# Kernel optimization log

Measured on AMD Instinct MI355X. Metric: run time of the kernel, lower is better.

## Reference

```python
import math
import jax, jax.numpy as jnp
import numpy as np

FACTOR = 5


def setup_inputs() -> dict:
    key = jax.random.key(0)
    kq, kk, kv, ki = jax.random.split(key, 4)
    B, H, L, D = 4, 8, 2048, 64
    sample_k = min(FACTOR * math.ceil(math.log(L)), L)  # 40
    queries = jax.random.normal(kq, (B, H, L, D), dtype=jnp.float32)
    keys = jax.random.normal(kk, (B, H, L, D), dtype=jnp.float32)
    values = jax.random.normal(kv, (B, H, L, D), dtype=jnp.float32)
    index_sample = jax.random.randint(ki, (L, sample_k), 0, L, dtype=jnp.int64 if jax.config.jax_enable_x64 else jnp.int32)
    return {"queries": queries, "keys": keys, "values": values, "index_sample": index_sample}


def reference(queries, keys, values, index_sample):
    B, H, L_Q, D = queries.shape
    L_K = keys.shape[2]
    u = min(FACTOR * math.ceil(math.log(L_Q)), L_Q)  # n_top queries (= 40)
    scale = 1.0 / math.sqrt(D)

    # --- _prob_QK: sparsity measurement over randomly sampled keys ---
    # K_sample[b,h,q,s,:] = keys[b,h,index_sample[q,s],:]  -> [B,H,L_Q,S,D]
    K_sample = keys[:, :, index_sample, :]
    Q_K_sample = jnp.einsum('bhqd,bhqsd->bhqs', queries, K_sample)  # [B,H,L_Q,S]
    M = Q_K_sample.max(axis=-1) - Q_K_sample.sum(axis=-1) / L_K      # [B,H,L_Q]
    _, M_top = jax.lax.top_k(M, u)                                    # [B,H,u]

    Q_reduce = jnp.take_along_axis(queries, M_top[..., None], axis=2)  # [B,H,u,D]
    scores_top = jnp.einsum('bhud,bhkd->bhuk', Q_reduce, keys) * scale  # [B,H,u,L_K]

    # --- initial context: causal cumulative sum of V (mask_flag=True) ---
    context = jnp.cumsum(values, axis=2)  # [B,H,L_Q,D]

    # --- ProbMask: causal rows gathered at the selected query indices ---
    causal = jnp.triu(jnp.ones((L_Q, L_K), dtype=bool), 1)  # [L_Q,L_K]
    mask = causal[M_top]                                     # [B,H,u,L_K]
    scores_top = jnp.where(mask, -jnp.inf, scores_top)

    attn = jax.nn.softmax(scores_top, axis=-1)                       # [B,H,u,L_K]
    update = jnp.einsum('bhuk,bhkd->bhud', attn, values)             # [B,H,u,D]

    b_idx = jnp.arange(B)[:, None, None]
    h_idx = jnp.arange(H)[None, :, None]
    context = context.at[b_idx, h_idx, M_top].set(update.astype(context.dtype))
    return context
```

## Files before the change

kernel.cpp:

```cpp
#include <hip/hip_runtime.h>
#include <math.h>

#define BB 4
#define HH 8
#define LL 2048
#define DD 64
#define SK 40
#define BH (BB*HH)

__device__ __forceinline__ unsigned ordu(float v) {
    unsigned u = __float_as_uint(v);
    return (u & 0x80000000u) ? ~u : (u | 0x80000000u);
}

__global__ __launch_bounds__(256) void stage1_kernel(
        const float* __restrict__ Q, const float* __restrict__ K,
        const float* __restrict__ V, const int* __restrict__ IDX,
        float* __restrict__ M, float* __restrict__ csum) {
    int tid = threadIdx.x;
    if (blockIdx.x < 1024) {
        int x = blockIdx.x;
        int bhLo = x & 7;
        int r = x >> 3;
        int bhHi = r & 3;
        int chunk = r >> 2;
        int bh = bhHi * 8 + bhLo;
        int qbase = chunk * 64;
        int w = tid >> 6, lane = tid & 63;
        int qw = lane >> 2, c = lane & 3;
        int qi = w * 16 + qw;
        int qpos = qbase + qi;

        __shared__ int sidx[64 * SK];
        for (int i = tid; i < 64 * SK; i += 256) sidx[i] = IDX[(size_t)qbase * SK + i];

        const float4* Q4 = (const float4*)Q;
        const float4* K4 = (const float4*)K;
        float4 qreg[4];
        #pragma unroll
        for (int j = 0; j < 4; ++j)
            qreg[j] = Q4[((size_t)bh * LL + qpos) * 16 + j * 4 + c];
        __syncthreads();

        size_t kb4 = (size_t)bh * LL * 16;
        float mx = -INFINITY, sm = 0.f;
        #pragma unroll 8
        for (int s = 0; s < SK; ++s) {
            int ks = sidx[qi * SK + s];
            const float4* kr = K4 + kb4 + (size_t)ks * 16;
            float p = 0.f;
            #pragma unroll
            for (int j = 0; j < 4; ++j) {
                float4 kv = kr[j * 4 + c];
                p += qreg[j].x * kv.x + qreg[j].y * kv.y + qreg[j].z * kv.z + qreg[j].w * kv.w;
            }
            p += __shfl_xor(p, 1, 64);
            p += __shfl_xor(p, 2, 64);
            mx = fmaxf(mx, p);
            sm += p;
        }
        if (c == 0) M[(size_t)bh * LL + qpos] = mx - sm * (1.0f / (float)LL);
    } else {
        int x = blockIdx.x - 1024;
        int bhLo = x & 7, r = x >> 3;
        int bhHi = r & 3, c = r >> 2;
        int bh = bhHi * 8 + bhLo;
        int d = tid & 63, sg = tid >> 6;
        size_t base = (size_t)bh * LL * DD;
        int row0 = c * 128 + sg * 32;
        float s = 0.f;
        for (int j = 0; j < 32; ++j) s += V[base + (size_t)(row0 + j) * DD + d];
        __shared__ float part[4][DD];
        part[sg][d] = s;
        __syncthreads();
        if (sg == 0)
            csum[((size_t)bh * 16 + c) * DD + d] = part[0][d] + part[1][d] + part[2][d] + part[3][d];
    }
}

__global__ __launch_bounds__(256) void stage2_kernel(
        const float* __restrict__ V, const float* __restrict__ csum,
        const float* __restrict__ M, float* __restrict__ out,
        int* __restrict__ topk) {
    int tid = threadIdx.x;
    if (blockIdx.x < 512) {
        int x = blockIdx.x;
        int bhLo = x & 7, r = x >> 3;
        int bhHi = r & 3, c = r >> 2;
        int bh = bhHi * 8 + bhLo;
        int d = tid & 63, sg = tid >> 6;
        size_t base = (size_t)bh * LL * DD;
        int row0 = c * 128 + sg * 32;
        float v[32];
        #pragma unroll
        for (int j = 0; j < 32; ++j) v[j] = V[base + (size_t)(row0 + j) * DD + d];
        float s = 0.f;
        #pragma unroll
        for (int j = 0; j < 32; ++j) s += v[j];
        __shared__ float part[4][DD];
        part[sg][d] = s;
        __syncthreads();
        float pre = 0.f;
        for (int cc = 0; cc < c; ++cc) pre += csum[((size_t)bh * 16 + cc) * DD + d];
        for (int ss = 0; ss < sg; ++ss) pre += part[ss][d];
        float acc = pre;
        #pragma unroll
        for (int j = 0; j < 32; ++j) {
            acc += v[j];
            out[base + (size_t)(row0 + j) * DD + d] = acc;
        }
    } else {
        int bh = blockIdx.x - 512;
        __shared__ unsigned hist[256];
        __shared__ unsigned bc_prefix, bc_need;
        __shared__ unsigned cnt_gt, cnt_eq;
        __shared__ int eqlist[128];

        unsigned v[8];
        #pragma unroll
        for (int j = 0; j < 8; ++j)
            v[j] = ordu(M[(size_t)bh * LL + tid + j * 256]);

        unsigned prefix = 0, need = SK;
        #pragma unroll
        for (int pass = 0; pass < 4; ++pass) {
            const int s = 24 - 8 * pass;
            const unsigned maskHigh = (pass == 0) ? 0u : (0xFFFFFFFFu << (s + 8));
            hist[tid] = 0;
            __syncthreads();
            #pragma unroll
            for (int j = 0; j < 8; ++j)
                if (((v[j] ^ prefix) & maskHigh) == 0)
                    atomicAdd(&hist[(v[j] >> s) & 0xFF], 1u);
            __syncthreads();
            unsigned above = 0;
            for (int b = tid + 1; b < 256; ++b) above += hist[b];
            if (above < need && above + hist[tid] >= need) {
                bc_prefix = prefix | ((unsigned)tid << s);
                bc_need = need - above;
            }
            __syncthreads();
            prefix = bc_prefix;
            need = bc_need;
            __syncthreads();
        }
        unsigned T = prefix;
        if (tid == 0) { cnt_gt = 0; cnt_eq = 0; }
        __syncthreads();
        #pragma unroll
        for (int j = 0; j < 8; ++j) {
            int idx = tid + j * 256;
            if (v[j] > T) { unsigned p = atomicAdd(&cnt_gt, 1u); topk[bh * SK + p] = idx; }
            else if (v[j] == T) { unsigned p = atomicAdd(&cnt_eq, 1u); if (p < 128) eqlist[p] = idx; }
        }
        __syncthreads();
        if (tid == 0) {
            int ne = (int)min(cnt_eq, 128u);
            unsigned base = cnt_gt;
            for (unsigned r2 = 0; r2 < need; ++r2) {
                int bj = 0, bv = 0x7FFFFFFF;
                for (int j = 0; j < ne; ++j)
                    if (eqlist[j] < bv) { bv = eqlist[j]; bj = j; }
                topk[bh * SK + base + r2] = bv;
                eqlist[bj] = 0x7FFFFFFF;
            }
        }
    }
}

__global__ __launch_bounds__(256) void attn_kernel(
        const float* __restrict__ Q, const float* __restrict__ K,
        const float* __restrict__ V, const int* __restrict__ topk,
        float* __restrict__ out) {
    int x = blockIdx.x;
    int bhLo = x & 7;
    int t = x >> 3;
    int u = t % SK;
    int bhHi = t / SK;
    int bh = bhHi * 8 + bhLo;
    int tid = threadIdx.x;

    int qpos = topk[bh * SK + u];
    int nk = qpos + 1;

    const float4* Q4 = (const float4*)Q;
    const float4* K4 = (const float4*)K;
    const float4* V4 = (const float4*)V;

    int w = tid >> 6, lane = tid & 63;
    int kw = lane >> 2, c = lane & 3;
    float4 qreg[4];
    #pragma unroll
    for (int j = 0; j < 4; ++j)
        qreg[j] = Q4[((size_t)bh * LL + qpos) * 16 + j * 4 + c];

    __shared__ float sc[LL];
    __shared__ float red[4], red2[4];
    __shared__ float opart[16][16][4];

    size_t kb4 = (size_t)bh * LL * 16;
    int rounds = (nk + 63) >> 6;
    for (int rr = 0; rr < rounds; ++rr) {
        int key = rr * 64 + w * 16 + kw;
        if (key < nk) {
            const float4* kr = K4 + kb4 + (size_t)key * 16;
            float p = 0.f;
            #pragma unroll
            for (int j = 0; j < 4; ++j) {
                float4 kv = kr[j * 4 + c];
                p += qreg[j].x * kv.x + qreg[j].y * kv.y + qreg[j].z * kv.z + qreg[j].w * kv.w;
            }
            p += __shfl_xor(p, 1, 64);
            p += __shfl_xor(p, 2, 64);
            if (c == 0) sc[key] = p * 0.125f;
        }
    }
    __syncthreads();

    float m = -INFINITY;
    for (int j = tid; j < nk; j += 256) m = fmaxf(m, sc[j]);
    #pragma unroll
    for (int off = 32; off > 0; off >>= 1) m = fmaxf(m, __shfl_xor(m, off, 64));
    if (lane == 0) red[w] = m;
    __syncthreads();
    m = fmaxf(fmaxf(red[0], red[1]), fmaxf(red[2], red[3]));

    float ls = 0.f;
    for (int j = tid; j < nk; j += 256) {
        float e = expf(sc[j] - m);
        sc[j] = e;
        ls += e;
    }
    #pragma unroll
    for (int off = 32; off > 0; off >>= 1) ls += __shfl_xor(ls, off, 64);
    if (lane == 0) red2[w] = ls;
    __syncthreads();
    float linv = 1.0f / (red2[0] + red2[1] + red2[2] + red2[3]);

    int col4 = tid & 15, kg = tid >> 4;
    float ax = 0.f, ay = 0.f, az = 0.f, aw = 0.f;
    for (int j = kg; j < nk; j += 16) {
        float sj = sc[j];
        float4 vv = V4[((size_t)bh * LL + j) * 16 + col4];
        ax += sj * vv.x; ay += sj * vv.y; az += sj * vv.z; aw += sj * vv.w;
    }
    opart[kg][col4][0] = ax;
    opart[kg][col4][1] = ay;
    opart[kg][col4][2] = az;
    opart[kg][col4][3] = aw;
    __syncthreads();
    if (tid < DD) {
        int c4 = tid >> 2, cp = tid & 3;
        float s = 0.f;
        #pragma unroll
        for (int kg2 = 0; kg2 < 16; ++kg2) s += opart[kg2][c4][cp];
        out[((size_t)bh * LL + qpos) * DD + tid] = s * linv;
    }
}

extern "C" void kernel_launch(void* const* d_in, const int* in_sizes, int n_in,
                              void* d_out, int out_size, void* d_ws, size_t ws_size,
                              hipStream_t stream) {
    const float* Q   = (const float*)d_in[0];
    const float* K   = (const float*)d_in[1];
    const float* V   = (const float*)d_in[2];
    const int*   IDX = (const int*)d_in[3];
    float* out = (float*)d_out;

    char* ws = (char*)d_ws;
    float* M    = (float*)ws;  ws += (size_t)BH * LL * sizeof(float);
    int*   topk = (int*)ws;    ws += ((size_t)BH * SK * sizeof(int) + 255) & ~255ull;
    float* csum = (float*)ws;

    stage1_kernel<<<1536, 256, 0, stream>>>(Q, K, V, IDX, M, csum);
    stage2_kernel<<<544, 256, 0, stream>>>(V, csum, M, out, topk);
    attn_kernel<<<BH * SK, 256, 0, stream>>>(Q, K, V, topk, out);
}
```

Measured before the change: 166.5 us.

## Software-prefetch K and V rows and reorder top-k output and attention grid

Adds register double-buffering of gathered K rows in the sparsity measurement loop, processing two samples per iteration so loads overlap the dot products. The attention kernel likewise prefetches the next K row and keeps a two-deep prefetch pipeline for V rows. Top-k indices are now written in descending position order through a shared rank sort, and the attention grid maps bh to the low bits, presumably to balance long and short causal rows across blocks. The cost is extra register pressure, which may lower occupancy.

```diff
diff --git a/kernel.cpp b/kernel.cpp
--- a/kernel.cpp
+++ b/kernel.cpp
@@ -43,21 +43,42 @@
         __syncthreads();
 
         size_t kb4 = (size_t)bh * LL * 16;
+        const int* myidx = sidx + qi * SK;
+
+        int iA = myidx[0], iB = myidx[1];
+        float4 A[4], B[4];
+        #pragma unroll
+        for (int j = 0; j < 4; ++j) {
+            A[j] = K4[kb4 + (size_t)iA * 16 + j * 4 + c];
+            B[j] = K4[kb4 + (size_t)iB * 16 + j * 4 + c];
+        }
+        int iC = myidx[2], iD = myidx[3];
+
         float mx = -INFINITY, sm = 0.f;
-        #pragma unroll 8
-        for (int s = 0; s < SK; ++s) {
-            int ks = sidx[qi * SK + s];
-            const float4* kr = K4 + kb4 + (size_t)ks * 16;
-            float p = 0.f;
+        for (int s = 0; s < SK; s += 2) {
+            float4 Cr[4], Dr[4];
+            if (s + 2 < SK) {
+                #pragma unroll
+                for (int j = 0; j < 4; ++j) {
+                    Cr[j] = K4[kb4 + (size_t)iC * 16 + j * 4 + c];
+                    Dr[j] = K4[kb4 + (size_t)iD * 16 + j * 4 + c];
+                }
+                if (s + 4 < SK) { iC = myidx[s + 4]; iD = myidx[s + 5]; }
+            }
+            float p0 = 0.f, p1 = 0.f;
             #pragma unroll
             for (int j = 0; j < 4; ++j) {
-                float4 kv = kr[j * 4 + c];
-                p += qreg[j].x * kv.x + qreg[j].y * kv.y + qreg[j].z * kv.z + qreg[j].w * kv.w;
+                p0 += A[j].x * qreg[j].x + A[j].y * qreg[j].y + A[j].z * qreg[j].z + A[j].w * qreg[j].w;
+                p1 += B[j].x * qreg[j].x + B[j].y * qreg[j].y + B[j].z * qreg[j].z + B[j].w * qreg[j].w;
             }
-            p += __shfl_xor(p, 1, 64);
-            p += __shfl_xor(p, 2, 64);
-            mx = fmaxf(mx, p);
-            sm += p;
+            p0 += __shfl_xor(p0, 1, 64);
+            p0 += __shfl_xor(p0, 2, 64);
+            p1 += __shfl_xor(p1, 1, 64);
+            p1 += __shfl_xor(p1, 2, 64);
+            mx = fmaxf(mx, fmaxf(p0, p1));
+            sm += p0 + p1;
+            #pragma unroll
+            for (int j = 0; j < 4; ++j) { A[j] = Cr[j]; B[j] = Dr[j]; }
         }
         if (c == 0) M[(size_t)bh * LL + qpos] = mx - sm * (1.0f / (float)LL);
     } else {
@@ -115,6 +136,7 @@
         __shared__ unsigned bc_prefix, bc_need;
         __shared__ unsigned cnt_gt, cnt_eq;
         __shared__ int eqlist[128];
+        __shared__ int sel[SK];
 
         unsigned v[8];
         #pragma unroll
@@ -150,7 +172,7 @@
         #pragma unroll
         for (int j = 0; j < 8; ++j) {
             int idx = tid + j * 256;
-            if (v[j] > T) { unsigned p = atomicAdd(&cnt_gt, 1u); topk[bh * SK + p] = idx; }
+            if (v[j] > T) { unsigned p = atomicAdd(&cnt_gt, 1u); sel[p] = idx; }
             else if (v[j] == T) { unsigned p = atomicAdd(&cnt_eq, 1u); if (p < 128) eqlist[p] = idx; }
         }
         __syncthreads();
@@ -161,9 +183,17 @@
                 int bj = 0, bv = 0x7FFFFFFF;
                 for (int j = 0; j < ne; ++j)
                     if (eqlist[j] < bv) { bv = eqlist[j]; bj = j; }
-                topk[bh * SK + base + r2] = bv;
+                sel[base + r2] = bv;
                 eqlist[bj] = 0x7FFFFFFF;
             }
+        }
+        __syncthreads();
+        if (tid < SK) {
+            int mine = sel[tid];
+            int rank = 0;
+            #pragma unroll
+            for (int j = 0; j < SK; ++j) rank += (sel[j] > mine);
+            topk[bh * SK + rank] = mine;
         }
     }
 }
@@ -173,11 +203,8 @@
         const float* __restrict__ V, const int* __restrict__ topk,
         float* __restrict__ out) {
     int x = blockIdx.x;
-    int bhLo = x & 7;
-    int t = x >> 3;
-    int u = t % SK;
-    int bhHi = t / SK;
-    int bh = bhHi * 8 + bhLo;
+    int bh = x & 31;
+    int u = x >> 5;
     int tid = threadIdx.x;
 
     int qpos = topk[bh * SK + u];
@@ -200,20 +227,31 @@
 
     size_t kb4 = (size_t)bh * LL * 16;
     int rounds = (nk + 63) >> 6;
+    int key0 = w * 16 + kw;
+    float4 A[4];
+    if (key0 < nk) {
+        #pragma unroll
+        for (int j = 0; j < 4; ++j) A[j] = K4[kb4 + (size_t)key0 * 16 + j * 4 + c];
+    }
     for (int rr = 0; rr < rounds; ++rr) {
-        int key = rr * 64 + w * 16 + kw;
+        int key = rr * 64 + key0;
+        int keyn = key + 64;
+        float4 B[4];
+        if (rr + 1 < rounds && keyn < nk) {
+            #pragma unroll
+            for (int j = 0; j < 4; ++j) B[j] = K4[kb4 + (size_t)keyn * 16 + j * 4 + c];
+        }
         if (key < nk) {
-            const float4* kr = K4 + kb4 + (size_t)key * 16;
             float p = 0.f;
             #pragma unroll
-            for (int j = 0; j < 4; ++j) {
-                float4 kv = kr[j * 4 + c];
-                p += qreg[j].x * kv.x + qreg[j].y * kv.y + qreg[j].z * kv.z + qreg[j].w * kv.w;
-            }
+            for (int j = 0; j < 4; ++j)
+                p += A[j].x * qreg[j].x + A[j].y * qreg[j].y + A[j].z * qreg[j].z + A[j].w * qreg[j].w;
             p += __shfl_xor(p, 1, 64);
             p += __shfl_xor(p, 2, 64);
             if (c == 0) sc[key] = p * 0.125f;
         }
+        #pragma unroll
+        for (int j = 0; j < 4; ++j) A[j] = B[j];
     }
     __syncthreads();
 
@@ -239,10 +277,17 @@
 
     int col4 = tid & 15, kg = tid >> 4;
     float ax = 0.f, ay = 0.f, az = 0.f, aw = 0.f;
+    size_t vb4 = (size_t)bh * LL * 16;
+    float4 Va = make_float4(0.f, 0.f, 0.f, 0.f);
+    float4 Vb = make_float4(0.f, 0.f, 0.f, 0.f);
+    if (kg < nk)      Va = V4[vb4 + (size_t)kg * 16 + col4];
+    if (kg + 16 < nk) Vb = V4[vb4 + (size_t)(kg + 16) * 16 + col4];
     for (int j = kg; j < nk; j += 16) {
+        float4 Vc = make_float4(0.f, 0.f, 0.f, 0.f);
+        if (j + 32 < nk) Vc = V4[vb4 + (size_t)(j + 32) * 16 + col4];
         float sj = sc[j];
-        float4 vv = V4[((size_t)bh * LL + j) * 16 + col4];
-        ax += sj * vv.x; ay += sj * vv.y; az += sj * vv.z; aw += sj * vv.w;
+        ax += sj * Va.x; ay += sj * Va.y; az += sj * Va.z; aw += sj * Va.w;
+        Va = Vb; Vb = Vc;
     }
     opart[kg][col4][0] = ax;
     opart[kg][col4][1] = ay;
```

After: 169.0 us. About the same (+1.5%).

## Split cumsum into finer chunks with float4 access and sort topk for attention scheduling

Applied to the files above, without the earlier changes.

Divides the cumulative-sum work into 32 chunks of 64 rows per head instead of 16 of 128, using float4 loads and stores with 16 row-groups per block, which doubles the cumsum block count in both stages. The top-k selection is now staged in shared memory and written out in descending index order. The attention grid is remapped so that blocks with the same rank across all heads are adjacent, which puts the longest causal rows first. This aims at better load balance and more memory-level parallelism, at the cost of longer serial prefix loops over chunk sums for later chunks.

```diff
diff --git a/kernel.cpp b/kernel.cpp
--- a/kernel.cpp
+++ b/kernel.cpp
@@ -7,10 +7,15 @@
 #define DD 64
 #define SK 40
 #define BH (BB*HH)
+#define NC 32
 
 __device__ __forceinline__ unsigned ordu(float v) {
     unsigned u = __float_as_uint(v);
     return (u & 0x80000000u) ? ~u : (u | 0x80000000u);
+}
+
+__device__ __forceinline__ float dot4(float4 a, float4 b) {
+    return a.x * b.x + a.y * b.y + a.z * b.z + a.w * b.w;
 }
 
 __global__ __launch_bounds__(256) void stage1_kernel(
@@ -18,6 +23,9 @@
         const float* __restrict__ V, const int* __restrict__ IDX,
         float* __restrict__ M, float* __restrict__ csum) {
     int tid = threadIdx.x;
+    __shared__ int sidx[64 * SK];
+    __shared__ float4 part4[16][16];
+
     if (blockIdx.x < 1024) {
         int x = blockIdx.x;
         int bhLo = x & 7;
@@ -31,7 +39,6 @@
         int qi = w * 16 + qw;
         int qpos = qbase + qi;
 
-        __shared__ int sidx[64 * SK];
         for (int i = tid; i < 64 * SK; i += 256) sidx[i] = IDX[(size_t)qbase * SK + i];
 
         const float4* Q4 = (const float4*)Q;
@@ -48,12 +55,8 @@
         for (int s = 0; s < SK; ++s) {
             int ks = sidx[qi * SK + s];
             const float4* kr = K4 + kb4 + (size_t)ks * 16;
-            float p = 0.f;
-            #pragma unroll
-            for (int j = 0; j < 4; ++j) {
-                float4 kv = kr[j * 4 + c];
-                p += qreg[j].x * kv.x + qreg[j].y * kv.y + qreg[j].z * kv.z + qreg[j].w * kv.w;
-            }
+            float p = dot4(kr[c], qreg[0]) + dot4(kr[4 + c], qreg[1])
+                    + dot4(kr[8 + c], qreg[2]) + dot4(kr[12 + c], qreg[3]);
             p += __shfl_xor(p, 1, 64);
             p += __shfl_xor(p, 2, 64);
             mx = fmaxf(mx, p);
@@ -65,16 +68,27 @@
         int bhLo = x & 7, r = x >> 3;
         int bhHi = r & 3, c = r >> 2;
         int bh = bhHi * 8 + bhLo;
-        int d = tid & 63, sg = tid >> 6;
-        size_t base = (size_t)bh * LL * DD;
-        int row0 = c * 128 + sg * 32;
-        float s = 0.f;
-        for (int j = 0; j < 32; ++j) s += V[base + (size_t)(row0 + j) * DD + d];
-        __shared__ float part[4][DD];
-        part[sg][d] = s;
-        __syncthreads();
-        if (sg == 0)
-            csum[((size_t)bh * 16 + c) * DD + d] = part[0][d] + part[1][d] + part[2][d] + part[3][d];
+        int col4 = tid & 15, sg = tid >> 4;
+        const float4* V4 = (const float4*)V;
+        size_t vb4 = (size_t)bh * LL * 16;
+        int row0 = c * 64 + sg * 4;
+        float4 s = make_float4(0.f, 0.f, 0.f, 0.f);
+        #pragma unroll
+        for (int j = 0; j < 4; ++j) {
+            float4 v = V4[vb4 + (size_t)(row0 + j) * 16 + col4];
+            s.x += v.x; s.y += v.y; s.z += v.z; s.w += v.w;
+        }
+        part4[sg][col4] = s;
+        __syncthreads();
+        if (tid < 16) {
+            float4 t = part4[0][tid];
+            #pragma unroll
+            for (int ss = 1; ss < 16; ++ss) {
+                float4 p = part4[ss][tid];
+                t.x += p.x; t.y += p.y; t.z += p.z; t.w += p.w;
+            }
+            ((float4*)csum)[((size_t)bh * NC + c) * 16 + tid] = t;
+        }
     }
 }
 
@@ -83,38 +97,53 @@
         const float* __restrict__ M, float* __restrict__ out,
         int* __restrict__ topk) {
     int tid = threadIdx.x;
-    if (blockIdx.x < 512) {
+    if (blockIdx.x < 1024) {
         int x = blockIdx.x;
         int bhLo = x & 7, r = x >> 3;
         int bhHi = r & 3, c = r >> 2;
         int bh = bhHi * 8 + bhLo;
-        int d = tid & 63, sg = tid >> 6;
-        size_t base = (size_t)bh * LL * DD;
-        int row0 = c * 128 + sg * 32;
-        float v[32];
-        #pragma unroll
-        for (int j = 0; j < 32; ++j) v[j] = V[base + (size_t)(row0 + j) * DD + d];
-        float s = 0.f;
-        #pragma unroll
-        for (int j = 0; j < 32; ++j) s += v[j];
-        __shared__ float part[4][DD];
-        part[sg][d] = s;
-        __syncthreads();
-        float pre = 0.f;
-        for (int cc = 0; cc < c; ++cc) pre += csum[((size_t)bh * 16 + cc) * DD + d];
-        for (int ss = 0; ss < sg; ++ss) pre += part[ss][d];
-        float acc = pre;
-        #pragma unroll
-        for (int j = 0; j < 32; ++j) {
-            acc += v[j];
-            out[base + (size_t)(row0 + j) * DD + d] = acc;
+        int col4 = tid & 15, sg = tid >> 4;
+        const float4* V4 = (const float4*)V;
+        const float4* C4 = (const float4*)csum;
+        float4* O4 = (float4*)out;
+        size_t vb4 = (size_t)bh * LL * 16;
+        int row0 = c * 64 + sg * 4;
+
+        float4 v[4];
+        #pragma unroll
+        for (int j = 0; j < 4; ++j)
+            v[j] = V4[vb4 + (size_t)(row0 + j) * 16 + col4];
+
+        __shared__ float4 part4[16][16];
+        float4 s = make_float4(v[0].x + v[1].x + v[2].x + v[3].x,
+                               v[0].y + v[1].y + v[2].y + v[3].y,
+                               v[0].z + v[1].z + v[2].z + v[3].z,
+                               v[0].w + v[1].w + v[2].w + v[3].w);
+        part4[sg][col4] = s;
+        __syncthreads();
+
+        float4 pre = make_float4(0.f, 0.f, 0.f, 0.f);
+        for (int cc = 0; cc < c; ++cc) {
+            float4 p = C4[((size_t)bh * NC + cc) * 16 + col4];
+            pre.x += p.x; pre.y += p.y; pre.z += p.z; pre.w += p.w;
+        }
+        for (int ss = 0; ss < sg; ++ss) {
+            float4 p = part4[ss][col4];
+            pre.x += p.x; pre.y += p.y; pre.z += p.z; pre.w += p.w;
+        }
+        float4 acc = pre;
+        #pragma unroll
+        for (int j = 0; j < 4; ++j) {
+            acc.x += v[j].x; acc.y += v[j].y; acc.z += v[j].z; acc.w += v[j].w;
+            O4[vb4 + (size_t)(row0 + j) * 16 + col4] = acc;
         }
     } else {
-        int bh = blockIdx.x - 512;
+        int bh = blockIdx.x - 1024;
         __shared__ unsigned hist[256];
         __shared__ unsigned bc_prefix, bc_need;
         __shared__ unsigned cnt_gt, cnt_eq;
         __shared__ int eqlist[128];
+        __shared__ int sel[SK];
 
         unsigned v[8];
         #pragma unroll
@@ -150,7 +179,7 @@
         #pragma unroll
         for (int j = 0; j < 8; ++j) {
             int idx = tid + j * 256;
-            if (v[j] > T) { unsigned p = atomicAdd(&cnt_gt, 1u); topk[bh * SK + p] = idx; }
+            if (v[j] > T) { unsigned p = atomicAdd(&cnt_gt, 1u); sel[p] = idx; }
             else if (v[j] == T) { unsigned p = atomicAdd(&cnt_eq, 1u); if (p < 128) eqlist[p] = idx; }
         }
         __syncthreads();
@@ -161,9 +190,17 @@
                 int bj = 0, bv = 0x7FFFFFFF;
                 for (int j = 0; j < ne; ++j)
                     if (eqlist[j] < bv) { bv = eqlist[j]; bj = j; }
-                topk[bh * SK + base + r2] = bv;
+                sel[base + r2] = bv;
                 eqlist[bj] = 0x7FFFFFFF;
             }
+        }
+        __syncthreads();
+        if (tid < SK) {
+            int mine = sel[tid];
+            int rank = 0;
+            #pragma unroll
+            for (int j = 0; j < SK; ++j) rank += (sel[j] > mine);
+            topk[bh * SK + rank] = mine;
         }
     }
 }
@@ -173,11 +210,8 @@
         const float* __restrict__ V, const int* __restrict__ topk,
         float* __restrict__ out) {
     int x = blockIdx.x;
-    int bhLo = x & 7;
-    int t = x >> 3;
-    int u = t % SK;
-    int bhHi = t / SK;
-    int bh = bhHi * 8 + bhLo;
+    int bh = x & 31;
+    int u = x >> 5;
     int tid = threadIdx.x;
 
     int qpos = topk[bh * SK + u];
@@ -204,12 +238,8 @@
         int key = rr * 64 + w * 16 + kw;
         if (key < nk) {
             const float4* kr = K4 + kb4 + (size_t)key * 16;
-            float p = 0.f;
-            #pragma unroll
-            for (int j = 0; j < 4; ++j) {
-                float4 kv = kr[j * 4 + c];
-                p += qreg[j].x * kv.x + qreg[j].y * kv.y + qreg[j].z * kv.z + qreg[j].w * kv.w;
-            }
+            float p = dot4(kr[c], qreg[0]) + dot4(kr[4 + c], qreg[1])
+                    + dot4(kr[8 + c], qreg[2]) + dot4(kr[12 + c], qreg[3]);
             p += __shfl_xor(p, 1, 64);
             p += __shfl_xor(p, 2, 64);
             if (c == 0) sc[key] = p * 0.125f;
@@ -239,9 +269,10 @@
 
     int col4 = tid & 15, kg = tid >> 4;
     float ax = 0.f, ay = 0.f, az = 0.f, aw = 0.f;
+    size_t vb4 = (size_t)bh * LL * 16;
     for (int j = kg; j < nk; j += 16) {
         float sj = sc[j];
-        float4 vv = V4[((size_t)bh * LL + j) * 16 + col4];
+        float4 vv = V4[vb4 + (size_t)j * 16 + col4];
         ax += sj * vv.x; ay += sj * vv.y; az += sj * vv.z; aw += sj * vv.w;
     }
     opart[kg][col4][0] = ax;
@@ -272,7 +303,7 @@
     int*   topk = (int*)ws;    ws += ((size_t)BH * SK * sizeof(int) + 255) & ~255ull;
     float* csum = (float*)ws;
 
-    stage1_kernel<<<1536, 256, 0, stream>>>(Q, K, V, IDX, M, csum);
-    stage2_kernel<<<544, 256, 0, stream>>>(V, csum, M, out, topk);
+    stage1_kernel<<<2048, 256, 0, stream>>>(Q, K, V, IDX, M, csum);
+    stage2_kernel<<<1056, 256, 0, stream>>>(V, csum, M, out, topk);
     attn_kernel<<<BH * SK, 256, 0, stream>>>(Q, K, V, topk, out);
 }
```

New measurement: 166.7 us. No clear change (+0.1%).
